# Optimization experiments

Measured on AMD Instinct MI355X. Metric: run time of the kernel, lower is better.

## Reference

```python
import jax, jax.numpy as jnp
import numpy as np
from jax import lax

# --- RPN config (eval / TEST path) ---
ASPECT = (0.5, 1.0, 2.0)
SCALE = (8.0, 16.0, 32.0)
STRIDE = 16
N_ANCHORS = len(ASPECT) * len(SCALE)  # 9
PRE_NMS = 6000
POST_NMS = 300
NMS_THRESH = 0.7
MIN_SIZE = 16.0
NEG = jnp.float32(-1e9)


def conv2d(x, w, b, pad):
    y = lax.conv_general_dilated(x, w, (1, 1), [(pad, pad), (pad, pad)],
                                 dimension_numbers=('NCHW', 'OIHW', 'NCHW'))
    return y + b[None, :, None, None]


def make_anchors(h, w):
    asp = jnp.array(ASPECT, jnp.float32)
    sc = jnp.array(SCALE, jnp.float32)
    size = float(STRIDE * STRIDE)
    ws = (jnp.sqrt(size / asp)[:, None] * sc[None, :]).reshape(-1)  # (A,)
    hs = (jnp.sqrt(size * asp)[:, None] * sc[None, :]).reshape(-1)
    c = (STRIDE - 1) / 2.0
    base = jnp.stack([c - 0.5 * (ws - 1), c - 0.5 * (hs - 1),
                      c + 0.5 * (ws - 1), c + 0.5 * (hs - 1)], axis=-1)  # (A,4)
    sx = jnp.arange(w, dtype=jnp.float32) * STRIDE
    sy = jnp.arange(h, dtype=jnp.float32) * STRIDE
    shift_x, shift_y = jnp.meshgrid(sx, sy)  # (h,w)
    shifts = jnp.stack([shift_x, shift_y, shift_x, shift_y], axis=-1)  # (h,w,4)
    return (shifts[:, :, None, :] + base[None, None]).reshape(-1, 4)  # (h*w*A,4)


def decode_boxes(anchors, deltas):
    wa = anchors[..., 2] - anchors[..., 0] + 1.0
    ha = anchors[..., 3] - anchors[..., 1] + 1.0
    cxa = anchors[..., 0] + 0.5 * wa
    cya = anchors[..., 1] + 0.5 * ha
    cx = deltas[..., 0] * wa + cxa
    cy = deltas[..., 1] * ha + cya
    pw = jnp.exp(deltas[..., 2]) * wa
    ph = jnp.exp(deltas[..., 3]) * ha
    return jnp.stack([cx - 0.5 * pw, cy - 0.5 * ph,
                      cx + 0.5 * pw, cy + 0.5 * ph], axis=-1)


def iou_one_many(box, boxes):
    x1 = jnp.maximum(box[0], boxes[:, 0])
    y1 = jnp.maximum(box[1], boxes[:, 1])
    x2 = jnp.minimum(box[2], boxes[:, 2])
    y2 = jnp.minimum(box[3], boxes[:, 3])
    inter = jnp.maximum(0.0, x2 - x1 + 1.0) * jnp.maximum(0.0, y2 - y1 + 1.0)
    a0 = (box[2] - box[0] + 1.0) * (box[3] - box[1] + 1.0)
    a1 = (boxes[:, 2] - boxes[:, 0] + 1.0) * (boxes[:, 3] - boxes[:, 1] + 1.0)
    return inter / (a0 + a1 - inter)


def nms_keep(boxes, scores):
    # boxes: (PRE,4) sorted by score desc; returns POST_NMS kept indices
    n = boxes.shape[0]

    def body(i, carry):
        valid, keep = carry
        s = jnp.where(valid, scores, NEG)
        j = jnp.argmax(s).astype(jnp.int32)
        keep = keep.at[i].set(j)
        iou = iou_one_many(boxes[j], boxes)
        valid = valid & (iou <= NMS_THRESH)
        valid = valid.at[j].set(False)
        return valid, keep

    _, keep = lax.fori_loop(0, POST_NMS, body,
                            (jnp.ones(n, bool), jnp.zeros(POST_NMS, jnp.int32)))
    return keep


def rpn_forward(input, im_info, w_feat, b_feat, w_cls, b_cls, w_reg, b_reg):
    feat = jax.nn.relu(conv2d(input, w_feat, b_feat, 1))  # (B,512,h,w)
    cls = conv2d(feat, w_cls, b_cls, 0)                    # (B,2A,h,w)
    B, _, h, w = cls.shape
    prob = jax.nn.softmax(cls.reshape(B, N_ANCHORS, 2, h, w), axis=2)
    fg = prob[:, :, 1]                                     # (B,A,h,w)
    scores = fg.transpose(0, 2, 3, 1).reshape(B, h * w * N_ANCHORS)
    reg = conv2d(feat, w_reg, b_reg, 0)                    # (B,4A,h,w)
    deltas = reg.transpose(0, 2, 3, 1).reshape(B, h * w * N_ANCHORS, 4)

    anchors = make_anchors(h, w)                           # (K,4)
    boxes = decode_boxes(anchors[None], deltas)            # (B,K,4)

    # clip to image
    im_h = im_info[:, 0][:, None]
    im_w = im_info[:, 1][:, None]
    x1 = jnp.clip(boxes[..., 0], 0.0, im_w - 1.0)
    y1 = jnp.clip(boxes[..., 1], 0.0, im_h - 1.0)
    x2 = jnp.clip(boxes[..., 2], 0.0, im_w - 1.0)
    y2 = jnp.clip(boxes[..., 3], 0.0, im_h - 1.0)
    boxes = jnp.stack([x1, y1, x2, y2], axis=-1)

    # min-size filter (mask scores instead of dropping rows)
    ms = MIN_SIZE * im_info[:, 2][:, None]
    ok = ((x2 - x1 + 1.0) >= ms) & ((y2 - y1 + 1.0) >= ms)
    scores = jnp.where(ok, scores, NEG)

    top_scores, order = lax.top_k(scores, PRE_NMS)         # (B,PRE)
    boxes_sorted = jnp.take_along_axis(boxes, order[..., None], axis=1)
    keep = jax.vmap(nms_keep)(boxes_sorted, top_scores)    # (B,POST)
    rois_boxes = jnp.take_along_axis(boxes_sorted, keep[..., None], axis=1)
    bidx = jnp.broadcast_to(jnp.arange(B, dtype=boxes.dtype)[:, None, None],
                            (B, POST_NMS, 1))
    return jnp.concatenate([bidx, rois_boxes], axis=-1)    # (B,POST,5)


def setup_inputs() -> dict:
    key = jax.random.key(0)
    ks = jax.random.split(key, 8)
    B, C, H, W = 8, 512, 64, 64
    inp = {
        'input': jax.random.normal(ks[0], (B, C, H, W), jnp.float32),
        'gt_box': jnp.zeros((B, 20, 5), jnp.float32),
        'im_info': jnp.tile(jnp.array([[1024.0, 1024.0, 1.0]], jnp.float32), (B, 1)),
        'w_feat': jax.random.normal(ks[1], (512, 512, 3, 3), jnp.float32) * 0.01,
        'b_feat': jnp.zeros((512,), jnp.float32),
        'w_cls': jax.random.normal(ks[2], (2 * N_ANCHORS, 512, 1, 1), jnp.float32) * 0.01,
        'b_cls': jnp.zeros((2 * N_ANCHORS,), jnp.float32),
        'w_reg': jax.random.normal(ks[3], (4 * N_ANCHORS, 512, 1, 1), jnp.float32) * 0.01,
        'b_reg': jnp.zeros((4 * N_ANCHORS,), jnp.float32),
    }
    return inp


def reference(input, gt_box, im_info, w_feat, b_feat, w_cls, b_cls, w_reg, b_reg):
    # eval-mode RPN: module returns (0, 0, rois); we return rois
    return rpn_forward(input, im_info, w_feat, b_feat, w_cls, b_cls, w_reg, b_reg)
```

## Files before the change

### kernel.cpp

```cpp
#include <hip/hip_runtime.h>
#include <hip/hip_bf16.h>
#include <stdint.h>

#define HW      64
#define CIN     512
#define KOUT    512
#define BATCH   8
#define NANCH   9
#define NBOX    (HW*HW*NANCH)
#define PRE_NMS 6000
#define POST_NMS 300
#define SORT_N  8192

__global__ __launch_bounds__(256, 2)
void conv3x3_relu(const float* __restrict__ in, const float* __restrict__ w,
                  const float* __restrict__ bias, float* __restrict__ feat) {
    __shared__ float s_in[8][6][68];
    __shared__ float s_w3[72 * 72];

    const int tid = threadIdx.x;
    const int k0  = blockIdx.x * 64;
    const int y0  = blockIdx.y * 4;
    const int b   = blockIdx.z;
    const int kg  = tid & 7;
    const int pos = tid >> 3;
    const int tx  = pos & 15;
    const int ty  = pos >> 4;
    const int x0  = tx * 4;

    float acc[2][8][4];
#pragma unroll
    for (int r = 0; r < 2; ++r)
#pragma unroll
        for (int k = 0; k < 8; ++k)
#pragma unroll
            for (int c = 0; c < 4; ++c) acc[r][k][c] = 0.0f;

    for (int cc = 0; cc < CIN; cc += 8) {
        __syncthreads();
        for (int i = tid; i < 8 * 6 * 66; i += 256) {
            int ci = i / 396; int rem = i % 396;
            int r = rem / 66; int col = rem % 66;
            int gx = col - 1; int gy = y0 - 1 + r;
            float v = 0.0f;
            if ((unsigned)gx < 64u && (unsigned)gy < 64u)
                v = in[(((size_t)b * CIN + cc + ci) * HW + gy) * HW + gx];
            s_in[ci][r][col] = v;
        }
        for (int i = tid; i < 64 * 72; i += 256) {
            int k = i / 72; int j = i % 72;
            s_w3[j * 72 + k] = w[(size_t)(k0 + k) * (CIN * 9) + cc * 9 + j];
        }
        __syncthreads();

#pragma unroll
        for (int ci = 0; ci < 8; ++ci) {
#pragma unroll
            for (int dy = 0; dy < 3; ++dy) {
                float iv[2][6];
#pragma unroll
                for (int rr = 0; rr < 2; ++rr) {
                    int r = ty * 2 + rr + dy;
                    float4 va = *(const float4*)&s_in[ci][r][x0];
                    float2 vb = *(const float2*)&s_in[ci][r][x0 + 4];
                    iv[rr][0] = va.x; iv[rr][1] = va.y; iv[rr][2] = va.z;
                    iv[rr][3] = va.w; iv[rr][4] = vb.x; iv[rr][5] = vb.y;
                }
#pragma unroll
                for (int dx = 0; dx < 3; ++dx) {
                    const float* wp = &s_w3[(ci * 9 + dy * 3 + dx) * 72 + kg * 8];
                    float4 w0v = *(const float4*)wp;
                    float4 w1v = *(const float4*)(wp + 4);
                    float wv[8] = {w0v.x, w0v.y, w0v.z, w0v.w,
                                   w1v.x, w1v.y, w1v.z, w1v.w};
#pragma unroll
                    for (int rr = 0; rr < 2; ++rr)
#pragma unroll
                        for (int k = 0; k < 8; ++k)
#pragma unroll
                            for (int c = 0; c < 4; ++c)
                                acc[rr][k][c] = fmaf(iv[rr][dx + c], wv[k], acc[rr][k][c]);
                }
            }
        }
    }
#pragma unroll
    for (int k = 0; k < 8; ++k) {
        float bv = bias[k0 + kg * 8 + k];
#pragma unroll
        for (int rr = 0; rr < 2; ++rr) {
            int y = y0 + ty * 2 + rr;
            float4 o;
            o.x = fmaxf(acc[rr][k][0] + bv, 0.0f);
            o.y = fmaxf(acc[rr][k][1] + bv, 0.0f);
            o.z = fmaxf(acc[rr][k][2] + bv, 0.0f);
            o.w = fmaxf(acc[rr][k][3] + bv, 0.0f);
            *(float4*)&feat[(((size_t)b * KOUT + k0 + kg * 8 + k) * HW + y) * HW + x0] = o;
        }
    }
}

__global__ __launch_bounds__(256, 2)
void heads(const float* __restrict__ feat,
           const float* __restrict__ wcls, const float* __restrict__ bcls,
           const float* __restrict__ wreg, const float* __restrict__ breg,
           const float* __restrict__ iminfo,
           unsigned long long* __restrict__ keys, float4* __restrict__ pbox) {
    __shared__ float s_w[128 * 56];

    const int tid = threadIdx.x;
    const int pix = blockIdx.x * 256 + tid;
    const int b   = pix >> 12;
    const int rem = pix & 4095;
    const int y   = rem >> 6;
    const int x   = rem & 63;

    float acc[54];
#pragma unroll
    for (int j = 0; j < 54; ++j) acc[j] = 0.0f;

    for (int cc = 0; cc < 512; cc += 128) {
        __syncthreads();
        for (int i = tid; i < 128 * 54; i += 256) {
            int j = i / 128; int cl = i % 128;
            float v = (j < 18) ? wcls[(size_t)j * 512 + cc + cl]
                               : wreg[(size_t)(j - 18) * 512 + cc + cl];
            s_w[cl * 56 + j] = v;
        }
        __syncthreads();
        for (int c2 = 0; c2 < 128; ++c2) {
            float f = feat[(((size_t)b * 512 + cc + c2) * 64 + y) * 64 + x];
#pragma unroll
            for (int j = 0; j < 54; ++j)
                acc[j] = fmaf(f, s_w[c2 * 56 + j], acc[j]);
        }
    }

    const float im_h = iminfo[b * 3 + 0];
    const float im_w = iminfo[b * 3 + 1];
    const float ms   = 16.0f * iminfo[b * 3 + 2];
    const float ASP[3] = {0.5f, 1.0f, 2.0f};
    const float SCL[3] = {8.0f, 16.0f, 32.0f};

#pragma unroll
    for (int a = 0; a < 9; ++a) {
        float c0 = acc[2 * a]     + bcls[2 * a];
        float c1 = acc[2 * a + 1] + bcls[2 * a + 1];
        float m  = fmaxf(c0, c1);
        float e0 = expf(c0 - m), e1 = expf(c1 - m);
        float fg = e1 / (e0 + e1);

        float d0 = acc[18 + 4 * a + 0] + breg[4 * a + 0];
        float d1 = acc[18 + 4 * a + 1] + breg[4 * a + 1];
        float d2 = acc[18 + 4 * a + 2] + breg[4 * a + 2];
        float d3 = acc[18 + 4 * a + 3] + breg[4 * a + 3];

        int ai = a / 3, si = a % 3;
        float wsz = sqrtf(256.0f / ASP[ai]) * SCL[si];
        float hsz = sqrtf(256.0f * ASP[ai]) * SCL[si];
        float sx = (float)x * 16.0f, sy = (float)y * 16.0f;
        float x1a = sx + (7.5f - 0.5f * (wsz - 1.0f));
        float y1a = sy + (7.5f - 0.5f * (hsz - 1.0f));
        float x2a = sx + (7.5f + 0.5f * (wsz - 1.0f));
        float y2a = sy + (7.5f + 0.5f * (hsz - 1.0f));

        float wa = x2a - x1a + 1.0f, ha = y2a - y1a + 1.0f;
        float cxa = x1a + 0.5f * wa, cya = y1a + 0.5f * ha;
        float cx = d0 * wa + cxa, cy = d1 * ha + cya;
        float pw = expf(d2) * wa, ph = expf(d3) * ha;
        float bx1 = cx - 0.5f * pw, by1 = cy - 0.5f * ph;
        float bx2 = cx + 0.5f * pw, by2 = cy + 0.5f * ph;

        bx1 = fminf(fmaxf(bx1, 0.0f), im_w - 1.0f);
        by1 = fminf(fmaxf(by1, 0.0f), im_h - 1.0f);
        bx2 = fminf(fmaxf(bx2, 0.0f), im_w - 1.0f);
        by2 = fminf(fmaxf(by2, 0.0f), im_h - 1.0f);

        bool ok = (bx2 - bx1 + 1.0f >= ms) && (by2 - by1 + 1.0f >= ms);
        float s = ok ? fg : -1e9f;

        unsigned u = __float_as_uint(s);
        u = (u & 0x80000000u) ? ~u : (u | 0x80000000u);
        int idx = (y * 64 + x) * 9 + a;
        keys[(size_t)b * NBOX + idx] =
            ((unsigned long long)u << 32) | (unsigned)(~(unsigned)idx);
        pbox[(size_t)b * NBOX + idx] = make_float4(bx1, by1, bx2, by2);
    }
}

__global__ __launch_bounds__(1024)
void select_sort(const unsigned long long* __restrict__ keys,
                 const float4* __restrict__ pbox,
                 float4* __restrict__ sorted) {
    __shared__ unsigned long long sbuf[SORT_N];
    __shared__ unsigned hist[16][256];
    __shared__ unsigned sh_prefix, sh_remaining, sh_counter;

    const int tid = threadIdx.x;
    const int b   = blockIdx.x;
    const int wv  = tid >> 6;
    const unsigned long long* kb = keys + (size_t)b * NBOX;

    if (tid == 0) { sh_prefix = 0u; sh_remaining = PRE_NMS; sh_counter = 0u; }

    for (int p = 3; p >= 0; --p) {
        for (int i = tid; i < 16 * 256; i += 1024) ((unsigned*)hist)[i] = 0u;
        __syncthreads();
        unsigned prefix = sh_prefix;
        unsigned pmask  = (p == 3) ? 0u : (0xFFFFFFFFu << (8 * (p + 1)));
        for (int i = tid; i < NBOX; i += 1024) {
            unsigned u = (unsigned)(kb[i] >> 32);
            if ((u & pmask) == prefix)
                atomicAdd(&hist[wv][(u >> (8 * p)) & 255], 1u);
        }
        __syncthreads();
        if (tid < 256) {
            unsigned s = 0;
#pragma unroll
            for (int w2 = 0; w2 < 16; ++w2) s += hist[w2][tid];
            hist[0][tid] = s;
        }
        __syncthreads();
        if (tid == 0) {
            unsigned rem = sh_remaining;
            int v = 255;
            for (; v > 0; --v) {
                unsigned c = hist[0][v];
                if (rem <= c) break;
                rem -= c;
            }
            sh_prefix    = prefix | ((unsigned)v << (8 * p));
            sh_remaining = rem;
        }
        __syncthreads();
    }
    const unsigned thr = sh_prefix;

    for (int i = tid; i < NBOX; i += 1024) {
        unsigned long long k = kb[i];
        bool act = ((unsigned)(k >> 32) >= thr);
        unsigned long long bal = __ballot(act);
        if (act) {
            int lane   = tid & 63;
            int leader = __ffsll(bal) - 1;
            unsigned base = 0;
            if (lane == leader) base = atomicAdd(&sh_counter, (unsigned)__popcll(bal));
            base = __shfl(base, leader);
            unsigned off = (unsigned)__popcll(bal & ((1ull << lane) - 1ull));
            unsigned pos2 = base + off;
            if (pos2 < SORT_N) sbuf[pos2] = k;
        }
    }
    __syncthreads();
    unsigned n = sh_counter; if (n > SORT_N) n = SORT_N;
    for (int i = (int)n + tid; i < SORT_N; i += 1024) sbuf[i] = 0ull;
    __syncthreads();

    for (int k = 2; k <= SORT_N; k <<= 1) {
        for (int j = k >> 1; j > 0; j >>= 1) {
            for (int t = tid; t < SORT_N / 2; t += 1024) {
                int i  = ((t & ~(j - 1)) << 1) | (t & (j - 1));
                int ix = i | j;
                bool up = ((i & k) == 0);
                unsigned long long a = sbuf[i], c = sbuf[ix];
                bool sw = up ? (a < c) : (a > c);
                if (sw) { sbuf[i] = c; sbuf[ix] = a; }
            }
            __syncthreads();
        }
    }

    for (int i = tid; i < PRE_NMS; i += 1024) {
        unsigned idx = ~((unsigned)sbuf[i]);
        sorted[(size_t)b * PRE_NMS + i] = pbox[(size_t)b * NBOX + idx];
    }
}

__global__ __launch_bounds__(512, 2)
void nms(const float4* __restrict__ sorted, float* __restrict__ out) {
    __shared__ unsigned long long vmask[94];
    __shared__ int sh_j;

    const int tid = threadIdx.x;
    const int b   = blockIdx.x;
    const float4* sb = sorted + (size_t)b * PRE_NMS;

    float4 bx[12]; float ar[12];
#pragma unroll
    for (int s = 0; s < 12; ++s) {
        int i = tid + 512 * s;
        if (i < PRE_NMS) {
            float4 v = sb[i];
            bx[s] = v;
            ar[s] = (v.z - v.x + 1.0f) * (v.w - v.y + 1.0f);
        } else {
            bx[s] = make_float4(0.f, 0.f, 0.f, 0.f);
            ar[s] = 1.0f;
        }
    }
    if (tid < 94) vmask[tid] = (tid < 93) ? ~0ull : ((1ull << 48) - 1ull);
    __syncthreads();

    for (int it = 0; it < POST_NMS; ++it) {
        if (tid < 64) {
            unsigned long long w0 = vmask[tid];
            unsigned long long w1 = (tid < 30) ? vmask[tid + 64] : 0ull;
            int cand = w0 ? (tid * 64 + __ffsll(w0) - 1)
                          : (w1 ? ((tid + 64) * 64 + __ffsll(w1) - 1) : 0x7FFFFFFF);
#pragma unroll
            for (int off = 32; off > 0; off >>= 1) {
                int o = __shfl_xor(cand, off);
                cand = (o < cand) ? o : cand;
            }
            if (tid == 0) sh_j = (cand == 0x7FFFFFFF) ? 0 : cand;
        }
        __syncthreads();
        int j = sh_j;
        float4 jb = sb[j];
        if (tid == 0) {
            float* o = out + ((size_t)b * POST_NMS + it) * 5;
            o[0] = (float)b; o[1] = jb.x; o[2] = jb.y; o[3] = jb.z; o[4] = jb.w;
        }
        float ja = (jb.z - jb.x + 1.0f) * (jb.w - jb.y + 1.0f);
#pragma unroll
        for (int s = 0; s < 12; ++s) {
            int i = tid + 512 * s;
            if (i < PRE_NMS && ((vmask[i >> 6] >> (i & 63)) & 1ull)) {
                float xx1 = fmaxf(jb.x, bx[s].x);
                float yy1 = fmaxf(jb.y, bx[s].y);
                float xx2 = fminf(jb.z, bx[s].z);
                float yy2 = fminf(jb.w, bx[s].w);
                float inter = fmaxf(0.0f, xx2 - xx1 + 1.0f) *
                              fmaxf(0.0f, yy2 - yy1 + 1.0f);
                float iou = inter / (ja + ar[s] - inter);
                if (iou > 0.7f)
                    atomicAnd(&vmask[i >> 6], ~(1ull << (i & 63)));
            }
        }
        __syncthreads();
    }
}

extern "C" void kernel_launch(void* const* d_in, const int* in_sizes, int n_in,
                              void* d_out, int out_size, void* d_ws, size_t ws_size,
                              hipStream_t stream) {
    (void)in_sizes; (void)n_in; (void)out_size; (void)ws_size;
    const float* input  = (const float*)d_in[0];
    const float* iminfo = (const float*)d_in[2];
    const float* wfeat  = (const float*)d_in[3];
    const float* bfeat  = (const float*)d_in[4];
    const float* wcls   = (const float*)d_in[5];
    const float* bcls   = (const float*)d_in[6];
    const float* wreg   = (const float*)d_in[7];
    const float* breg   = (const float*)d_in[8];
    float* out = (float*)d_out;

    char* ws = (char*)d_ws;
    float*               feat   = (float*)ws;
    unsigned long long*  keys   = (unsigned long long*)(ws + 67108864);
    float4*              pbox   = (float4*)(ws + 67108864 + 2359296);
    float4*              sorted = (float4*)(ws + 67108864 + 2359296 + 4718592);

    conv3x3_relu<<<dim3(8, 16, 8), 256, 0, stream>>>(input, wfeat, bfeat, feat);
    heads<<<dim3(128), 256, 0, stream>>>(feat, wcls, bcls, wreg, breg, iminfo, keys, pbox);
    select_sort<<<dim3(8), 1024, 0, stream>>>(keys, pbox, sorted);
    nms<<<dim3(8), 512, 0, stream>>>(sorted, out);
}
```

Before: 3.281 ms.

## Double-buffer conv3x3 shared tiles with register prefetch and vectorized loads

The 3x3 conv now keeps two LDS buffers for input and weight tiles. The next channel chunk is prefetched into registers with float4 global loads while the current chunk is computed, which removes one barrier per iteration and the scalar, divide-heavy load loops. Halo padding comes from zeroing LDS once up front, with boundary rows skipped. This raises LDS and register use, which could lower occupancy under the 2-block launch bound. The 1x1 head loop also gets an unroll-by-8 pragma.

After: 3.177 ms. 3.2% less time.

```diff
diff --git a/kernel.cpp b/kernel.cpp
--- a/kernel.cpp
+++ b/kernel.cpp
@@ -15,8 +15,8 @@
 __global__ __launch_bounds__(256, 2)
 void conv3x3_relu(const float* __restrict__ in, const float* __restrict__ w,
                   const float* __restrict__ bias, float* __restrict__ feat) {
-    __shared__ float s_in[8][6][68];
-    __shared__ float s_w3[72 * 72];
+    __shared__ float s_in[2][8][6][68];
+    __shared__ float s_w3[2][72 * 72];
 
     const int tid = threadIdx.x;
     const int k0  = blockIdx.x * 64;
@@ -28,6 +28,42 @@
     const int ty  = pos >> 4;
     const int x0  = tx * 4;
 
+    int in_lds[3]; int in_goff[3]; bool in_ok[3];
+#pragma unroll
+    for (int s = 0; s < 3; ++s) {
+        int v  = tid + 256 * s;
+        int ci = v / 96, rem = v % 96;
+        int r  = rem >> 4, c4 = rem & 15;
+        int gy = y0 - 1 + r;
+        in_ok[s]  = ((unsigned)gy < 64u);
+        int gyc   = gy < 0 ? 0 : (gy > 63 ? 63 : gy);
+        in_lds[s] = (ci * 6 + r) * 68 + 1 + 4 * c4;
+        in_goff[s] = ((b * 512 + ci) * 64 + gyc) * 64 + 4 * c4;
+    }
+    int w_lds[5]; int w_goff[5]; bool w_ok[5];
+#pragma unroll
+    for (int s = 0; s < 5; ++s) {
+        int q = tid + 256 * s;
+        w_ok[s] = (q < 1152);
+        int qq = w_ok[s] ? q : 0;
+        int k = qq / 18, j4 = qq % 18;
+        w_lds[s]  = (j4 * 4) * 72 + k;
+        w_goff[s] = (k0 + k) * 4608 + 4 * j4;
+    }
+
+    for (int i = tid; i < 2 * 8 * 6 * 68; i += 256) ((float*)s_in)[i] = 0.0f;
+
+    float4 pin[3], pw[5];
+    auto prefetch = [&](int ch) {
+#pragma unroll
+        for (int s = 0; s < 3; ++s)
+            pin[s] = *(const float4*)&in[in_goff[s] + ch * 4096];
+#pragma unroll
+        for (int s = 0; s < 5; ++s)
+            pw[s] = *(const float4*)&w[w_goff[s] + ch * 9];
+    };
+    prefetch(0);
+
     float acc[2][8][4];
 #pragma unroll
     for (int r = 0; r < 2; ++r)
@@ -36,22 +72,26 @@
 #pragma unroll
             for (int c = 0; c < 4; ++c) acc[r][k][c] = 0.0f;
 
-    for (int cc = 0; cc < CIN; cc += 8) {
-        __syncthreads();
-        for (int i = tid; i < 8 * 6 * 66; i += 256) {
-            int ci = i / 396; int rem = i % 396;
-            int r = rem / 66; int col = rem % 66;
-            int gx = col - 1; int gy = y0 - 1 + r;
-            float v = 0.0f;
-            if ((unsigned)gx < 64u && (unsigned)gy < 64u)
-                v = in[(((size_t)b * CIN + cc + ci) * HW + gy) * HW + gx];
-            s_in[ci][r][col] = v;
-        }
-        for (int i = tid; i < 64 * 72; i += 256) {
-            int k = i / 72; int j = i % 72;
-            s_w3[j * 72 + k] = w[(size_t)(k0 + k) * (CIN * 9) + cc * 9 + j];
-        }
-        __syncthreads();
+    for (int cc8 = 0; cc8 < 64; ++cc8) {
+        float* SIN = &s_in[cc8 & 1][0][0][0];
+        float* SW  = &s_w3[cc8 & 1][0];
+
+#pragma unroll
+        for (int s = 0; s < 3; ++s) if (in_ok[s]) {
+            SIN[in_lds[s] + 0] = pin[s].x;
+            SIN[in_lds[s] + 1] = pin[s].y;
+            SIN[in_lds[s] + 2] = pin[s].z;
+            SIN[in_lds[s] + 3] = pin[s].w;
+        }
+#pragma unroll
+        for (int s = 0; s < 5; ++s) if (w_ok[s]) {
+            SW[w_lds[s] + 0 * 72] = pw[s].x;
+            SW[w_lds[s] + 1 * 72] = pw[s].y;
+            SW[w_lds[s] + 2 * 72] = pw[s].z;
+            SW[w_lds[s] + 3 * 72] = pw[s].w;
+        }
+        __syncthreads();
+        if (cc8 < 63) prefetch((cc8 + 1) * 8);
 
 #pragma unroll
         for (int ci = 0; ci < 8; ++ci) {
@@ -61,14 +101,15 @@
 #pragma unroll
                 for (int rr = 0; rr < 2; ++rr) {
                     int r = ty * 2 + rr + dy;
-                    float4 va = *(const float4*)&s_in[ci][r][x0];
-                    float2 vb = *(const float2*)&s_in[ci][r][x0 + 4];
+                    const float* rowp = &SIN[(ci * 6 + r) * 68];
+                    float4 va = *(const float4*)&rowp[x0];
+                    float2 vb = *(const float2*)&rowp[x0 + 4];
                     iv[rr][0] = va.x; iv[rr][1] = va.y; iv[rr][2] = va.z;
                     iv[rr][3] = va.w; iv[rr][4] = vb.x; iv[rr][5] = vb.y;
                 }
 #pragma unroll
                 for (int dx = 0; dx < 3; ++dx) {
-                    const float* wp = &s_w3[(ci * 9 + dy * 3 + dx) * 72 + kg * 8];
+                    const float* wp = &SW[(ci * 9 + dy * 3 + dx) * 72 + kg * 8];
                     float4 w0v = *(const float4*)wp;
                     float4 w1v = *(const float4*)(wp + 4);
                     float wv[8] = {w0v.x, w0v.y, w0v.z, w0v.w,
@@ -128,6 +169,7 @@
             s_w[cl * 56 + j] = v;
         }
         __syncthreads();
+#pragma unroll 8
         for (int c2 = 0; c2 < 128; ++c2) {
             float f = feat[(((size_t)b * 512 + cc + c2) * 64 + y) * 64 + x];
 #pragma unroll
```
